# Kernel optimization log

Measured on AMD Instinct MI355X. Metric: run time of the kernel, lower is better.

Reference implementation:

```python
import jax, jax.numpy as jnp
import numpy as np

N, K, D = 65536, 8192, 256

def setup_inputs() -> dict:
    key = jax.random.key(0)
    k1, k2 = jax.random.split(key)
    z = jax.random.normal(k1, (N, D), dtype=jnp.float32)
    # torch init: uniform(-1/K, 1/K)
    emb_w = jax.random.uniform(k2, (K, D), dtype=jnp.float32, minval=-1.0 / K, maxval=1.0 / K)
    return {"z": z, "emb_w": emb_w}

def reference(z, emb_w):
    # distance[n,k] = ||z_n||^2 + ||e_k||^2 - 2 z_n . e_k  (argmin is gradient-free)
    z2 = jnp.sum(z * z, axis=1, keepdims=True)            # [N,1]
    e2 = jnp.sum(emb_w * emb_w, axis=1)                    # [K]
    distance = z2 + e2 - 2.0 * (z @ emb_w.T)               # [N,K]
    indices = jnp.argmin(distance, axis=-1)                # [N]
    quantized = emb_w[indices]                             # [N,D]
    straight_through = jax.lax.stop_gradient(quantized - z) + z
    return quantized, straight_through, indices
```

## Files before the change

### kernel.cpp

```cpp
#include <hip/hip_runtime.h>
#include <hip/hip_fp16.h>

#define N_TOK 65536
#define K_EMB 8192
#define D_DIM 256
#define LIST_CAP 12288
#define CAND_CAP 16384

typedef unsigned short u16;
typedef unsigned int u32;
typedef unsigned long long u64;
typedef _Float16 f16x8 __attribute__((ext_vector_type(8)));
typedef float f32x16 __attribute__((ext_vector_type(16)));

__device__ __forceinline__ u16 f2h(float f) {
  union { _Float16 h; u16 u; } c; c.h = (_Float16)f; return c.u;
}
__device__ __forceinline__ f16x8 as_f16x8(uint4 v) {
  union { uint4 u; f16x8 h; } c; c.u = v; return c.h;
}
__device__ __forceinline__ void gld_lds16(const u16* g, u16* l) {
  __builtin_amdgcn_global_load_lds((const __attribute__((address_space(1))) void*)g,
                                   (__attribute__((address_space(3))) void*)l,
                                   16, 0, 0);
}

__global__ void vq_prep(const float* __restrict__ emb, u16* __restrict__ ehh,
                        float* __restrict__ e2f, u16* __restrict__ e2h,
                        int* __restrict__ count, int* __restrict__ candcount) {
  if (blockIdx.x == 0 && threadIdx.x == 0) { *count = 0; *candcount = 0; }
  const int w = threadIdx.x >> 6, lane = threadIdx.x & 63;
  const int k = blockIdx.x * 4 + w;
  const float4 v = ((const float4*)(emb + (size_t)k * D_DIM))[lane];
  uint2 p;
  p.x = (u32)f2h(v.x * 524288.0f) | ((u32)f2h(v.y * 524288.0f) << 16);
  p.y = (u32)f2h(v.z * 524288.0f) | ((u32)f2h(v.w * 524288.0f) << 16);
  ((uint2*)(ehh + (size_t)k * D_DIM))[lane] = p;
  double s = (double)v.x * v.x + (double)v.y * v.y +
             (double)v.z * v.z + (double)v.w * v.w;
  #pragma unroll
  for (int off = 32; off > 0; off >>= 1) s += __shfl_down(s, off);
  if (lane == 0) { e2f[k] = (float)s; e2h[k] = f2h(-(float)s * 16777216.0f); }
}

__global__ void vq_z2(const float* __restrict__ zg, float* __restrict__ z2f) {
  const int w = threadIdx.x >> 6, lane = threadIdx.x & 63;
  const int n = blockIdx.x * 4 + w;
  const float4 v = ((const float4*)(zg + (size_t)n * D_DIM))[lane];
  double s = (double)v.x * v.x + (double)v.y * v.y +
             (double)v.z * v.z + (double)v.w * v.w;
  #pragma unroll
  for (int off = 32; off > 0; off >>= 1) s += __shfl_down(s, off);
  if (lane == 0) z2f[n] = (float)s;
}

__launch_bounds__(512, 4)
__global__ void vq_phase1(const float* __restrict__ zg, const u16* __restrict__ ehh,
                          const u16* __restrict__ e2h, const float* __restrict__ z2f,
                          int* __restrict__ idx1_ws, int* __restrict__ thrbuf,
                          u64* __restrict__ refbuf, int* __restrict__ list,
                          int* __restrict__ count) {
  __shared__ u16 lds[2][16384];

  const int tid  = threadIdx.x;
  const int w    = tid >> 6;
  const int lane = tid & 63;
  const int q    = w & 1;
  const int g    = w >> 1;
  const int col  = lane & 31;
  const int h    = lane >> 5;
  const int n0   = blockIdx.x * 128 + g * 32;

  uint4 zres[16];
  {
    const float4* zp = (const float4*)(zg + (size_t)(n0 + col) * D_DIM);
    #pragma unroll
    for (int c = 0; c < 16; ++c) {
      float4 a = zp[c * 4 + h * 2];
      float4 b = zp[c * 4 + h * 2 + 1];
      uint4 u;
      u.x = (u32)f2h(a.x * 64.0f) | ((u32)f2h(a.y * 64.0f) << 16);
      u.y = (u32)f2h(a.z * 64.0f) | ((u32)f2h(a.w * 64.0f) << 16);
      u.z = (u32)f2h(b.x * 64.0f) | ((u32)f2h(b.y * 64.0f) << 16);
      u.w = (u32)f2h(b.z * 64.0f) | ((u32)f2h(b.w * 64.0f) << 16);
      zres[c] = u;
    }
  }
  uint4 bone = {0, 0, 0, 0};
  if (h == 0) bone.x = 0x3C00u;

  int m1 = (int)0x80000000, m2 = (int)0x80000000;

  #pragma unroll
  for (int i = 0; i < 4; ++i) {
    int pp = w * 4 + i, qs = pp >> 4, cs = pp & 15;
    gld_lds16(ehh + (size_t)(qs * 32 + col) * D_DIM + cs * 16 + h * 8,
              &lds[0][qs * 8192 + cs * 512]);
  }

  for (int t = 0; t < 128; ++t) {
    const int b = t & 1;
    __syncthreads();
    if (t + 1 < 128) {
      const int nb = b ^ 1, kb2 = (t + 1) * 64;
      #pragma unroll
      for (int i = 0; i < 4; ++i) {
        int pp = w * 4 + i, qs = pp >> 4, cs = pp & 15;
        gld_lds16(ehh + (size_t)(kb2 + qs * 32 + col) * D_DIM + cs * 16 + h * 8,
                  &lds[nb][qs * 8192 + cs * 512]);
      }
    }
    const int kb = t * 64 + q * 32;
    uint4 ea = {0, 0, 0, 0};
    if (h == 0) ea.x = (u32)e2h[kb + col];

    const u16* lb = &lds[b][q * 8192];
    f32x16 acc = {};
    #pragma unroll
    for (int c = 0; c < 16; ++c) {
      f16x8 a = as_f16x8(*(const uint4*)(lb + c * 512 + lane * 8));
      acc = __builtin_amdgcn_mfma_f32_32x32x16_f16(a, as_f16x8(zres[c]), acc, 0, 0, 0);
    }
    acc = __builtin_amdgcn_mfma_f32_32x32x16_f16(as_f16x8(ea), as_f16x8(bone), acc, 0, 0, 0);

    const int base_inv = 4095 - t * 32 - q * 16;
    #pragma unroll
    for (int r = 0; r < 16; ++r) {
      int key = ((int)acc[r] << 12) + (base_inv - r);
      m2 = max(m2, min(m1, key));
      m1 = max(m1, key);
    }
  }

  int k1;
  {
    int x = 4095 - (m1 & 4095);
    int kt = x >> 5, kq = (x >> 4) & 1, kr = x & 15;
    k1 = kt * 64 + kq * 32 + (kr & 3) + 8 * (kr >> 2) + 4 * h;
    int o1 = __shfl_xor(m1, 32), o2 = __shfl_xor(m2, 32);
    int ok1 = __shfl_xor(k1, 32);
    bool take = (o1 > m1) || (o1 == m1 && ok1 < k1);
    int loser = take ? m1 : o1;
    if (take) { m1 = o1; k1 = ok1; }
    m2 = max(m2, max(o2, loser));
  }

  __syncthreads();
  int* rm1 = (int*)&lds[0][0];
  int* rk1 = (int*)&lds[0][1024];
  int* rm2 = (int*)&lds[0][2048];
  if (lane < 32) {
    int nl = q * 128 + g * 32 + col;
    rm1[nl] = m1; rk1[nl] = k1; rm2[nl] = m2;
  }
  __syncthreads();
  if (tid < 128) {
    int a1 = rm1[tid], a2 = rm2[tid], ak = rk1[tid];
    int c1 = rm1[128 + tid], c2 = rm2[128 + tid], ck = rk1[128 + tid];
    bool take = (c1 > a1) || (c1 == a1 && ck < ak);
    int M1 = take ? c1 : a1;
    int K1 = take ? ck : ak;
    int M2 = max(max(a2, c2), take ? a1 : c1);
    int n = blockIdx.x * 128 + tid;
    int M1a = M1 >> 12, M2a = M2 >> 12;
    int e = (int)((__float_as_uint(z2f[n] + 0.01f) >> 23) & 255);
    e = min(max(e, 127), 140);
    int bin = 1 << (e - 126);
    int p = 0;
    if ((M1a - M2a) < (bin * 2 + 128)) {
      int pos = atomicAdd(count, 1);
      if (pos < LIST_CAP) {
        list[pos] = n;
        thrbuf[pos] = M1a - (bin + 256);
        refbuf[pos] = 0xFFFFFFFFFFFFFFFFULL;
        p = pos + 1;
      }
    }
    idx1_ws[n] = K1 | (p << 13);
  }
}

__launch_bounds__(512, 2)
__global__ void vq_cand(const float* __restrict__ zg, const u16* __restrict__ ehh,
                        const u16* __restrict__ e2h, const int* __restrict__ count,
                        const int* __restrict__ list, const int* __restrict__ thrbuf,
                        u32* __restrict__ candbuf, int* __restrict__ candcount) {
  __shared__ u16 lds[2][32768];
  int cnt = *count; if (cnt > LIST_CAP) cnt = LIST_CAP;
  const int tile = blockIdx.x;
  if (tile * 64 >= cnt) return;
  const int tid = threadIdx.x, w = tid >> 6, lane = tid & 63;
  const int q = w & 3, g = w >> 2;
  const int col = lane & 31, h = lane >> 5;
  const int ct = tile * 64 + g * 32 + col;
  const bool valid = ct < cnt;
  const int n_tok = valid ? (list[ct] & (N_TOK - 1)) : 0;
  const int thr = valid ? thrbuf[ct] : 0x7FFFFFFF;

  uint4 zres[16];
  {
    const float4* zp = (const float4*)(zg + (size_t)n_tok * D_DIM);
    #pragma unroll
    for (int c = 0; c < 16; ++c) {
      float4 a = zp[c * 4 + h * 2];
      float4 b2 = zp[c * 4 + h * 2 + 1];
      uint4 u;
      u.x = (u32)f2h(a.x * 64.0f) | ((u32)f2h(a.y * 64.0f) << 16);
      u.y = (u32)f2h(a.z * 64.0f) | ((u32)f2h(a.w * 64.0f) << 16);
      u.z = (u32)f2h(b2.x * 64.0f) | ((u32)f2h(b2.y * 64.0f) << 16);
      u.w = (u32)f2h(b2.z * 64.0f) | ((u32)f2h(b2.w * 64.0f) << 16);
      zres[c] = u;
    }
  }
  uint4 bone = {0, 0, 0, 0};
  if (h == 0) bone.x = 0x3C00u;

  #pragma unroll
  for (int i = 0; i < 8; ++i) {
    int p2 = w * 8 + i, qs = p2 >> 4, cs = p2 & 15;
    gld_lds16(ehh + (size_t)(qs * 32 + col) * D_DIM + cs * 16 + h * 8,
              &lds[0][qs * 8192 + cs * 512]);
  }

  for (int tK = 0; tK < 64; ++tK) {
    const int b = tK & 1;
    __syncthreads();
    if (tK + 1 < 64) {
      const int nb = b ^ 1, kb2 = (tK + 1) * 128;
      #pragma unroll
      for (int i = 0; i < 8; ++i) {
        int p2 = w * 8 + i, qs = p2 >> 4, cs = p2 & 15;
        gld_lds16(ehh + (size_t)(kb2 + qs * 32 + col) * D_DIM + cs * 16 + h * 8,
                  &lds[nb][qs * 8192 + cs * 512]);
      }
    }
    const int kb = tK * 128 + q * 32;
    uint4 ea = {0, 0, 0, 0};
    if (h == 0) ea.x = (u32)e2h[kb + col];
    const u16* lb = &lds[b][q * 8192];
    f32x16 acc = {};
    #pragma unroll
    for (int c = 0; c < 16; ++c) {
      f16x8 a = as_f16x8(*(const uint4*)(lb + c * 512 + lane * 8));
      acc = __builtin_amdgcn_mfma_f32_32x32x16_f16(a, as_f16x8(zres[c]), acc, 0, 0, 0);
    }
    acc = __builtin_amdgcn_mfma_f32_32x32x16_f16(as_f16x8(ea), as_f16x8(bone), acc, 0, 0, 0);
    #pragma unroll
    for (int r = 0; r < 16; ++r) {
      if ((int)acc[r] >= thr) {
        int kg = kb + (r & 3) + 8 * (r >> 2) + 4 * h;
        int pos = atomicAdd(candcount, 1);
        if (pos < CAND_CAP) candbuf[pos] = ((u32)ct << 13) | (u32)kg;
      }
    }
  }
}

__global__ void vq_refine2(const float* __restrict__ zg, const float* __restrict__ emb,
                           const float* __restrict__ z2f, const float* __restrict__ e2f,
                           const int* __restrict__ list, const int* __restrict__ candcount,
                           const u32* __restrict__ candbuf, u64* __restrict__ refbuf) {
  const int w = threadIdx.x >> 6, lane = threadIdx.x & 63;
  int ccnt = *candcount; if (ccnt > CAND_CAP) ccnt = CAND_CAP;
  for (int i = blockIdx.x * 4 + w; i < ccnt; i += gridDim.x * 4) {
    const u32 rec = candbuf[i];
    const int p = (int)(rec >> 13), k = (int)(rec & 8191u);
    const int n = list[p] & (N_TOK - 1);
    float4 zv = ((const float4*)(zg + (size_t)n * D_DIM))[lane];
    float4 ev = ((const float4*)(emb + (size_t)k * D_DIM))[lane];
    double s = (double)zv.x * ev.x + (double)zv.y * ev.y +
               (double)zv.z * ev.z + (double)zv.w * ev.w;
    #pragma unroll
    for (int off = 32; off > 0; off >>= 1) s += __shfl_down(s, off);
    if (lane == 0) {
      float S = z2f[n] + e2f[k];
      float val = S - 2.0f * (float)s;
      u64 key = ((u64)__float_as_uint(val) << 13) | (u64)k;
      atomicMin((unsigned long long*)(refbuf + p), (unsigned long long)key);
    }
  }
}

__global__ void vq_gather(const float* __restrict__ emb, const int* __restrict__ idx1_ws,
                          const u64* __restrict__ refbuf, float* __restrict__ out) {
  const int w = threadIdx.x >> 6, lane = threadIdx.x & 63;
  const int n = blockIdx.x * 4 + w;
  const int enc = idx1_ws[n];
  int idx = enc & 8191;
  const int p = enc >> 13;
  if (p > 0) {
    u64 rb = refbuf[p - 1];
    if (rb != 0xFFFFFFFFFFFFFFFFULL) idx = (int)(rb & 8191ULL);
  }
  float4 v = ((const float4*)(emb + (size_t)idx * D_DIM))[lane];
  float4* o = (float4*)out;
  o[(size_t)n * 64 + lane] = v;
  o[(size_t)4194304 + (size_t)n * 64 + lane] = v;
  if (lane == 0) out[(size_t)33554432 + n] = (float)idx;
}

extern "C" void kernel_launch(void* const* d_in, const int* in_sizes, int n_in,
                              void* d_out, int out_size, void* d_ws, size_t ws_size,
                              hipStream_t stream) {
  const float* z   = (const float*)d_in[0];
  const float* emb = (const float*)d_in[1];
  char* ws = (char*)d_ws;
  u16*   ehh       = (u16*)(ws);
  float* e2f       = (float*)(ws + 4194304);
  u16*   e2h       = (u16*)(ws + 4227072);
  float* z2f       = (float*)(ws + 4243456);
  int*   idx1_ws   = (int*)(ws + 4505600);
  u64*   refbuf    = (u64*)(ws + 4767744);
  int*   list      = (int*)(ws + 4866048);
  int*   thrbuf    = (int*)(ws + 4915200);
  u32*   candbuf   = (u32*)(ws + 4964352);
  int*   count     = (int*)(ws + 5029888);
  int*   candcount = (int*)(ws + 5029892);

  vq_prep   <<<K_EMB / 4, 256, 0, stream>>>(emb, ehh, e2f, e2h, count, candcount);
  vq_z2     <<<N_TOK / 4, 256, 0, stream>>>(z, z2f);
  vq_phase1 <<<N_TOK / 128, 512, 0, stream>>>(z, ehh, e2h, z2f, idx1_ws, thrbuf,
                                              refbuf, list, count);
  vq_cand   <<<256, 512, 0, stream>>>(z, ehh, e2h, count, list, thrbuf,
                                      candbuf, candcount);
  vq_refine2<<<256, 256, 0, stream>>>(z, emb, z2f, e2f, list, candcount,
                                      candbuf, refbuf);
  vq_gather <<<N_TOK / 4, 256, 0, stream>>>(emb, idx1_ws, refbuf, (float*)d_out);
}
```

Before: 742.4 us.

## Fuse z-norm into phase1, software-pipeline its MFMA loop, split candidate K range

Removes the separate vq_z2 kernel by computing each token's squared norm in double while phase1 loads z. The norm is kept in LDS for the threshold test and also written to global memory for refine. The phase1 main loop now alternates two accumulators, so the argmax scan of one tile overlaps the MFMAs of the next. vq_cand splits the codebook into four K slices per row tile, raising its grid from 256 to 768 blocks, and refine2's grid is doubled. These changes add parallelism and cut a launch, at the cost of higher register pressure in phase1 and redundant z conversion across the K-split blocks.

```diff
diff --git a/kernel.cpp b/kernel.cpp
--- a/kernel.cpp
+++ b/kernel.cpp
@@ -43,24 +43,14 @@
   if (lane == 0) { e2f[k] = (float)s; e2h[k] = f2h(-(float)s * 16777216.0f); }
 }
 
-__global__ void vq_z2(const float* __restrict__ zg, float* __restrict__ z2f) {
-  const int w = threadIdx.x >> 6, lane = threadIdx.x & 63;
-  const int n = blockIdx.x * 4 + w;
-  const float4 v = ((const float4*)(zg + (size_t)n * D_DIM))[lane];
-  double s = (double)v.x * v.x + (double)v.y * v.y +
-             (double)v.z * v.z + (double)v.w * v.w;
-  #pragma unroll
-  for (int off = 32; off > 0; off >>= 1) s += __shfl_down(s, off);
-  if (lane == 0) z2f[n] = (float)s;
-}
-
 __launch_bounds__(512, 4)
 __global__ void vq_phase1(const float* __restrict__ zg, const u16* __restrict__ ehh,
-                          const u16* __restrict__ e2h, const float* __restrict__ z2f,
+                          const u16* __restrict__ e2h, float* __restrict__ z2f,
                           int* __restrict__ idx1_ws, int* __restrict__ thrbuf,
                           u64* __restrict__ refbuf, int* __restrict__ list,
                           int* __restrict__ count) {
   __shared__ u16 lds[2][16384];
+  __shared__ float z2s[128];
 
   const int tid  = threadIdx.x;
   const int w    = tid >> 6;
@@ -72,12 +62,17 @@
   const int n0   = blockIdx.x * 128 + g * 32;
 
   uint4 zres[16];
+  double zs = 0.0;
   {
     const float4* zp = (const float4*)(zg + (size_t)(n0 + col) * D_DIM);
     #pragma unroll
     for (int c = 0; c < 16; ++c) {
       float4 a = zp[c * 4 + h * 2];
       float4 b = zp[c * 4 + h * 2 + 1];
+      zs += (double)a.x * a.x + (double)a.y * a.y +
+            (double)a.z * a.z + (double)a.w * a.w;
+      zs += (double)b.x * b.x + (double)b.y * b.y +
+            (double)b.z * b.z + (double)b.w * b.w;
       uint4 u;
       u.x = (u32)f2h(a.x * 64.0f) | ((u32)f2h(a.y * 64.0f) << 16);
       u.y = (u32)f2h(a.z * 64.0f) | ((u32)f2h(a.w * 64.0f) << 16);
@@ -86,51 +81,74 @@
       zres[c] = u;
     }
   }
+  zs += __shfl_xor(zs, 32);
+  if (lane < 32) {
+    z2s[g * 32 + col] = (float)zs;
+    z2f[n0 + col] = (float)zs;
+  }
+
   uint4 bone = {0, 0, 0, 0};
   if (h == 0) bone.x = 0x3C00u;
 
   int m1 = (int)0x80000000, m2 = (int)0x80000000;
-
-  #pragma unroll
-  for (int i = 0; i < 4; ++i) {
-    int pp = w * 4 + i, qs = pp >> 4, cs = pp & 15;
-    gld_lds16(ehh + (size_t)(qs * 32 + col) * D_DIM + cs * 16 + h * 8,
-              &lds[0][qs * 8192 + cs * 512]);
-  }
-
-  for (int t = 0; t < 128; ++t) {
-    const int b = t & 1;
+  f32x16 accA = {}, accB = {};
+
+#define P1_STAGE(TT, BUF) { \
+    _Pragma("unroll") \
+    for (int i = 0; i < 4; ++i) { \
+      int pp = w * 4 + i, qs = pp >> 4, cs = pp & 15; \
+      gld_lds16(ehh + (size_t)((TT) * 64 + qs * 32 + col) * D_DIM + cs * 16 + h * 8, \
+                &lds[BUF][qs * 8192 + cs * 512]); \
+    } }
+#define P1_COMPUTE(ACC, TT, BUF) { \
+    const int kb_ = (TT) * 64 + q * 32; \
+    uint4 ea_ = {0, 0, 0, 0}; \
+    if (h == 0) ea_.x = (u32)e2h[kb_ + col]; \
+    const u16* lb_ = &lds[BUF][q * 8192]; \
+    _Pragma("unroll") \
+    for (int c = 0; c < 16; ++c) { \
+      f16x8 a_ = as_f16x8(*(const uint4*)(lb_ + c * 512 + lane * 8)); \
+      ACC = __builtin_amdgcn_mfma_f32_32x32x16_f16(a_, as_f16x8(zres[c]), ACC, 0, 0, 0); \
+    } \
+    ACC = __builtin_amdgcn_mfma_f32_32x32x16_f16(as_f16x8(ea_), as_f16x8(bone), ACC, 0, 0, 0); }
+#define P1_SCAN(ACC, TT) { \
+    const int base_inv_ = 4095 - (TT) * 32 - q * 16; \
+    _Pragma("unroll") \
+    for (int r = 0; r < 16; ++r) { \
+      int key_ = ((int)ACC[r] << 12) + (base_inv_ - r); \
+      m2 = max(m2, min(m1, key_)); \
+      m1 = max(m1, key_); \
+    } }
+#define P1_ZERO(ACC) { \
+    _Pragma("unroll") \
+    for (int r = 0; r < 16; ++r) ACC[r] = 0.0f; }
+
+  P1_STAGE(0, 0);
+  __syncthreads();
+  P1_STAGE(1, 1);
+  P1_COMPUTE(accA, 0, 0);
+
+  for (int t = 1; t < 127; t += 2) {
     __syncthreads();
-    if (t + 1 < 128) {
-      const int nb = b ^ 1, kb2 = (t + 1) * 64;
-      #pragma unroll
-      for (int i = 0; i < 4; ++i) {
-        int pp = w * 4 + i, qs = pp >> 4, cs = pp & 15;
-        gld_lds16(ehh + (size_t)(kb2 + qs * 32 + col) * D_DIM + cs * 16 + h * 8,
-                  &lds[nb][qs * 8192 + cs * 512]);
-      }
-    }
-    const int kb = t * 64 + q * 32;
-    uint4 ea = {0, 0, 0, 0};
-    if (h == 0) ea.x = (u32)e2h[kb + col];
-
-    const u16* lb = &lds[b][q * 8192];
-    f32x16 acc = {};
-    #pragma unroll
-    for (int c = 0; c < 16; ++c) {
-      f16x8 a = as_f16x8(*(const uint4*)(lb + c * 512 + lane * 8));
-      acc = __builtin_amdgcn_mfma_f32_32x32x16_f16(a, as_f16x8(zres[c]), acc, 0, 0, 0);
-    }
-    acc = __builtin_amdgcn_mfma_f32_32x32x16_f16(as_f16x8(ea), as_f16x8(bone), acc, 0, 0, 0);
-
-    const int base_inv = 4095 - t * 32 - q * 16;
-    #pragma unroll
-    for (int r = 0; r < 16; ++r) {
-      int key = ((int)acc[r] << 12) + (base_inv - r);
-      m2 = max(m2, min(m1, key));
-      m1 = max(m1, key);
-    }
-  }
+    P1_STAGE(t + 1, (t + 1) & 1);
+    P1_COMPUTE(accB, t, t & 1);
+    P1_SCAN(accA, t - 1);
+    P1_ZERO(accA);
+    __syncthreads();
+    P1_STAGE(t + 2, (t + 2) & 1);
+    P1_COMPUTE(accA, t + 1, (t + 1) & 1);
+    P1_SCAN(accB, t);
+    P1_ZERO(accB);
+  }
+  __syncthreads();
+  P1_COMPUTE(accB, 127, 1);
+  P1_SCAN(accA, 126);
+  P1_SCAN(accB, 127);
+
+#undef P1_STAGE
+#undef P1_COMPUTE
+#undef P1_SCAN
+#undef P1_ZERO
 
   int k1;
   {
@@ -163,7 +181,7 @@
     int M2 = max(max(a2, c2), take ? a1 : c1);
     int n = blockIdx.x * 128 + tid;
     int M1a = M1 >> 12, M2a = M2 >> 12;
-    int e = (int)((__float_as_uint(z2f[n] + 0.01f) >> 23) & 255);
+    int e = (int)((__float_as_uint(z2s[tid] + 0.01f) >> 23) & 255);
     e = min(max(e, 127), 140);
     int bin = 1 << (e - 126);
     int p = 0;
@@ -187,12 +205,14 @@
                         u32* __restrict__ candbuf, int* __restrict__ candcount) {
   __shared__ u16 lds[2][32768];
   int cnt = *count; if (cnt > LIST_CAP) cnt = LIST_CAP;
-  const int tile = blockIdx.x;
-  if (tile * 64 >= cnt) return;
+  const int rt = blockIdx.x >> 2;
+  const int ks = blockIdx.x & 3;
+  if (rt * 64 >= cnt) return;
+  const int k0 = ks * 2048;
   const int tid = threadIdx.x, w = tid >> 6, lane = tid & 63;
   const int q = w & 3, g = w >> 2;
   const int col = lane & 31, h = lane >> 5;
-  const int ct = tile * 64 + g * 32 + col;
+  const int ct = rt * 64 + g * 32 + col;
   const bool valid = ct < cnt;
   const int n_tok = valid ? (list[ct] & (N_TOK - 1)) : 0;
   const int thr = valid ? thrbuf[ct] : 0x7FFFFFFF;
@@ -218,15 +238,15 @@
   #pragma unroll
   for (int i = 0; i < 8; ++i) {
     int p2 = w * 8 + i, qs = p2 >> 4, cs = p2 & 15;
-    gld_lds16(ehh + (size_t)(qs * 32 + col) * D_DIM + cs * 16 + h * 8,
+    gld_lds16(ehh + (size_t)(k0 + qs * 32 + col) * D_DIM + cs * 16 + h * 8,
               &lds[0][qs * 8192 + cs * 512]);
   }
 
-  for (int tK = 0; tK < 64; ++tK) {
+  for (int tK = 0; tK < 16; ++tK) {
     const int b = tK & 1;
     __syncthreads();
-    if (tK + 1 < 64) {
-      const int nb = b ^ 1, kb2 = (tK + 1) * 128;
+    if (tK + 1 < 16) {
+      const int nb = b ^ 1, kb2 = k0 + (tK + 1) * 128;
       #pragma unroll
       for (int i = 0; i < 8; ++i) {
         int p2 = w * 8 + i, qs = p2 >> 4, cs = p2 & 15;
@@ -234,7 +254,7 @@
                   &lds[nb][qs * 8192 + cs * 512]);
       }
     }
-    const int kb = tK * 128 + q * 32;
+    const int kb = k0 + tK * 128 + q * 32;
     uint4 ea = {0, 0, 0, 0};
     if (h == 0) ea.x = (u32)e2h[kb + col];
     const u16* lb = &lds[b][q * 8192];
@@ -318,12 +338,11 @@
   int*   candcount = (int*)(ws + 5029892);
 
   vq_prep   <<<K_EMB / 4, 256, 0, stream>>>(emb, ehh, e2f, e2h, count, candcount);
-  vq_z2     <<<N_TOK / 4, 256, 0, stream>>>(z, z2f);
   vq_phase1 <<<N_TOK / 128, 512, 0, stream>>>(z, ehh, e2h, z2f, idx1_ws, thrbuf,
                                               refbuf, list, count);
-  vq_cand   <<<256, 512, 0, stream>>>(z, ehh, e2h, count, list, thrbuf,
+  vq_cand   <<<768, 512, 0, stream>>>(z, ehh, e2h, count, list, thrbuf,
                                       candbuf, candcount);
-  vq_refine2<<<256, 256, 0, stream>>>(z, emb, z2f, e2f, list, candcount,
+  vq_refine2<<<512, 256, 0, stream>>>(z, emb, z2f, e2f, list, candcount,
                                       candbuf, refbuf);
   vq_gather <<<N_TOK / 4, 256, 0, stream>>>(emb, idx1_ws, refbuf, (float*)d_out);
 }
```

Result: slower. 881.3 us (+18.7%).

## Make phase1 codebook-stationary with K-sliced partials and a merge pass

Applied to the files above, without the earlier changes.

Phase1 now has each block hold a 128-code slice of the fp16 codebook in LDS once. Blocks stream precomputed fp16 token rows and write per-slice top-2 partials to scratch, and a new merge kernel reduces them and builds the candidate list. This replaces the per-block double-buffered streaming of the whole codebook and the in-loop fp32→fp16 conversion of z. The candidate kernel is also split four ways over K for more parallelism, and the refine grid is enlarged. The trade-off is tens of MB of partial traffic, written into the output buffer as scratch, plus one extra launch.

```diff
diff --git a/kernel.cpp b/kernel.cpp
--- a/kernel.cpp
+++ b/kernel.cpp
@@ -6,6 +6,8 @@
 #define D_DIM 256
 #define LIST_CAP 12288
 #define CAND_CAP 16384
+#define NSLICE 64
+#define KSLICE 128
 
 typedef unsigned short u16;
 typedef unsigned int u32;
@@ -43,10 +45,15 @@
   if (lane == 0) { e2f[k] = (float)s; e2h[k] = f2h(-(float)s * 16777216.0f); }
 }
 
-__global__ void vq_z2(const float* __restrict__ zg, float* __restrict__ z2f) {
+__global__ void vq_zprep(const float* __restrict__ zg, u16* __restrict__ zhh,
+                         float* __restrict__ z2f) {
   const int w = threadIdx.x >> 6, lane = threadIdx.x & 63;
   const int n = blockIdx.x * 4 + w;
   const float4 v = ((const float4*)(zg + (size_t)n * D_DIM))[lane];
+  uint2 p;
+  p.x = (u32)f2h(v.x * 64.0f) | ((u32)f2h(v.y * 64.0f) << 16);
+  p.y = (u32)f2h(v.z * 64.0f) | ((u32)f2h(v.w * 64.0f) << 16);
+  ((uint2*)(zhh + (size_t)n * D_DIM))[lane] = p;
   double s = (double)v.x * v.x + (double)v.y * v.y +
              (double)v.z * v.z + (double)v.w * v.w;
   #pragma unroll
@@ -54,130 +61,121 @@
   if (lane == 0) z2f[n] = (float)s;
 }
 
-__launch_bounds__(512, 4)
-__global__ void vq_phase1(const float* __restrict__ zg, const u16* __restrict__ ehh,
-                          const u16* __restrict__ e2h, const float* __restrict__ z2f,
-                          int* __restrict__ idx1_ws, int* __restrict__ thrbuf,
-                          u64* __restrict__ refbuf, int* __restrict__ list,
-                          int* __restrict__ count) {
-  __shared__ u16 lds[2][16384];
+__launch_bounds__(512, 2)
+__global__ void vq_phase1(const u16* __restrict__ zhh, const u16* __restrict__ ehh,
+                          const u16* __restrict__ e2h,
+                          int* __restrict__ pm1, u32* __restrict__ pk,
+                          int* __restrict__ pm2) {
+  __shared__ u16 lds[32768];
 
   const int tid  = threadIdx.x;
   const int w    = tid >> 6;
   const int lane = tid & 63;
-  const int q    = w & 1;
-  const int g    = w >> 1;
   const int col  = lane & 31;
   const int h    = lane >> 5;
-  const int n0   = blockIdx.x * 128 + g * 32;
-
-  uint4 zres[16];
-  {
-    const float4* zp = (const float4*)(zg + (size_t)(n0 + col) * D_DIM);
-    #pragma unroll
-    for (int c = 0; c < 16; ++c) {
-      float4 a = zp[c * 4 + h * 2];
-      float4 b = zp[c * 4 + h * 2 + 1];
-      uint4 u;
-      u.x = (u32)f2h(a.x * 64.0f) | ((u32)f2h(a.y * 64.0f) << 16);
-      u.y = (u32)f2h(a.z * 64.0f) | ((u32)f2h(a.w * 64.0f) << 16);
-      u.z = (u32)f2h(b.x * 64.0f) | ((u32)f2h(b.y * 64.0f) << 16);
-      u.w = (u32)f2h(b.z * 64.0f) | ((u32)f2h(b.w * 64.0f) << 16);
-      zres[c] = u;
-    }
-  }
+  const int slice = blockIdx.x & (NSLICE - 1);
+  const int chunk = blockIdx.x >> 6;
+  const int k0    = slice * KSLICE;
+  const int nbase = chunk * 16384;
+
+  #pragma unroll
+  for (int i = 0; i < 8; ++i) {
+    int pp = w * 8 + i, qs = pp >> 4, cs = pp & 15;
+    gld_lds16(ehh + (size_t)(k0 + qs * 32 + col) * D_DIM + cs * 16 + h * 8,
+              &lds[qs * 8192 + cs * 512]);
+  }
+
   uint4 bone = {0, 0, 0, 0};
   if (h == 0) bone.x = 0x3C00u;
-
-  int m1 = (int)0x80000000, m2 = (int)0x80000000;
-
-  #pragma unroll
-  for (int i = 0; i < 4; ++i) {
-    int pp = w * 4 + i, qs = pp >> 4, cs = pp & 15;
-    gld_lds16(ehh + (size_t)(qs * 32 + col) * D_DIM + cs * 16 + h * 8,
-              &lds[0][qs * 8192 + cs * 512]);
-  }
-
-  for (int t = 0; t < 128; ++t) {
-    const int b = t & 1;
-    __syncthreads();
-    if (t + 1 < 128) {
-      const int nb = b ^ 1, kb2 = (t + 1) * 64;
+  uint4 ea[4] = {{0,0,0,0},{0,0,0,0},{0,0,0,0},{0,0,0,0}};
+  #pragma unroll
+  for (int kt = 0; kt < 4; ++kt)
+    if (h == 0) ea[kt].x = (u32)e2h[k0 + kt * 32 + col];
+
+  __syncthreads();
+
+  for (int it = 0; it < 64; ++it) {
+    const int n0 = nbase + it * 256 + w * 32;
+    const uint4* zp = (const uint4*)(zhh + (size_t)(n0 + col) * D_DIM);
+    uint4 zres[16];
+    #pragma unroll
+    for (int c = 0; c < 16; ++c) zres[c] = zp[c * 2 + h];
+
+    f32x16 acc[4] = {};
+    #pragma unroll
+    for (int c = 0; c < 16; ++c) {
+      f16x8 zb = as_f16x8(zres[c]);
       #pragma unroll
-      for (int i = 0; i < 4; ++i) {
-        int pp = w * 4 + i, qs = pp >> 4, cs = pp & 15;
-        gld_lds16(ehh + (size_t)(kb2 + qs * 32 + col) * D_DIM + cs * 16 + h * 8,
-                  &lds[nb][qs * 8192 + cs * 512]);
+      for (int kt = 0; kt < 4; ++kt) {
+        f16x8 a = as_f16x8(*(const uint4*)(&lds[kt * 8192 + c * 512 + lane * 8]));
+        acc[kt] = __builtin_amdgcn_mfma_f32_32x32x16_f16(a, zb, acc[kt], 0, 0, 0);
       }
     }
-    const int kb = t * 64 + q * 32;
-    uint4 ea = {0, 0, 0, 0};
-    if (h == 0) ea.x = (u32)e2h[kb + col];
-
-    const u16* lb = &lds[b][q * 8192];
-    f32x16 acc = {};
-    #pragma unroll
-    for (int c = 0; c < 16; ++c) {
-      f16x8 a = as_f16x8(*(const uint4*)(lb + c * 512 + lane * 8));
-      acc = __builtin_amdgcn_mfma_f32_32x32x16_f16(a, as_f16x8(zres[c]), acc, 0, 0, 0);
-    }
-    acc = __builtin_amdgcn_mfma_f32_32x32x16_f16(as_f16x8(ea), as_f16x8(bone), acc, 0, 0, 0);
-
-    const int base_inv = 4095 - t * 32 - q * 16;
-    #pragma unroll
-    for (int r = 0; r < 16; ++r) {
-      int key = ((int)acc[r] << 12) + (base_inv - r);
-      m2 = max(m2, min(m1, key));
-      m1 = max(m1, key);
-    }
-  }
-
-  int k1;
-  {
-    int x = 4095 - (m1 & 4095);
-    int kt = x >> 5, kq = (x >> 4) & 1, kr = x & 15;
-    k1 = kt * 64 + kq * 32 + (kr & 3) + 8 * (kr >> 2) + 4 * h;
+    #pragma unroll
+    for (int kt = 0; kt < 4; ++kt)
+      acc[kt] = __builtin_amdgcn_mfma_f32_32x32x16_f16(as_f16x8(ea[kt]),
+                                                       as_f16x8(bone), acc[kt], 0, 0, 0);
+
+    int m1 = (int)0x80000000, m2 = (int)0x80000000;
+    #pragma unroll
+    for (int kt = 0; kt < 4; ++kt) {
+      const int base_inv = 127 - kt * 32;
+      #pragma unroll
+      for (int r = 0; r < 16; ++r) {
+        int key = ((int)acc[kt][r] << 12) + (base_inv - ((r & 3) + 8 * (r >> 2)));
+        m2 = max(m2, min(m1, key));
+        m1 = max(m1, key);
+      }
+    }
+    int pos = 127 - (m1 & 4095);
+    int k1 = k0 + pos + 4 * h;
     int o1 = __shfl_xor(m1, 32), o2 = __shfl_xor(m2, 32);
     int ok1 = __shfl_xor(k1, 32);
     bool take = (o1 > m1) || (o1 == m1 && ok1 < k1);
     int loser = take ? m1 : o1;
     if (take) { m1 = o1; k1 = ok1; }
     m2 = max(m2, max(o2, loser));
-  }
-
-  __syncthreads();
-  int* rm1 = (int*)&lds[0][0];
-  int* rk1 = (int*)&lds[0][1024];
-  int* rm2 = (int*)&lds[0][2048];
-  if (lane < 32) {
-    int nl = q * 128 + g * 32 + col;
-    rm1[nl] = m1; rk1[nl] = k1; rm2[nl] = m2;
-  }
-  __syncthreads();
-  if (tid < 128) {
-    int a1 = rm1[tid], a2 = rm2[tid], ak = rk1[tid];
-    int c1 = rm1[128 + tid], c2 = rm2[128 + tid], ck = rk1[128 + tid];
-    bool take = (c1 > a1) || (c1 == a1 && ck < ak);
-    int M1 = take ? c1 : a1;
-    int K1 = take ? ck : ak;
-    int M2 = max(max(a2, c2), take ? a1 : c1);
-    int n = blockIdx.x * 128 + tid;
-    int M1a = M1 >> 12, M2a = M2 >> 12;
-    int e = (int)((__float_as_uint(z2f[n] + 0.01f) >> 23) & 255);
-    e = min(max(e, 127), 140);
-    int bin = 1 << (e - 126);
-    int p = 0;
-    if ((M1a - M2a) < (bin * 2 + 128)) {
-      int pos = atomicAdd(count, 1);
-      if (pos < LIST_CAP) {
-        list[pos] = n;
-        thrbuf[pos] = M1a - (bin + 256);
-        refbuf[pos] = 0xFFFFFFFFFFFFFFFFULL;
-        p = pos + 1;
-      }
-    }
-    idx1_ws[n] = K1 | (p << 13);
-  }
+
+    if (lane < 32) {
+      size_t idx = (size_t)slice * N_TOK + (n0 + col);
+      pm1[idx] = m1 >> 12;
+      pk[idx]  = (u32)k1;
+      pm2[idx] = m2 >> 12;
+    }
+  }
+}
+
+__global__ void vq_merge(const float* __restrict__ z2f, const int* __restrict__ pm1,
+                         const u32* __restrict__ pk, const int* __restrict__ pm2,
+                         int* __restrict__ idx1_ws, int* __restrict__ thrbuf,
+                         u64* __restrict__ refbuf, int* __restrict__ list,
+                         int* __restrict__ count) {
+  const int n = blockIdx.x * 256 + threadIdx.x;
+  int M1 = (int)0x80000000, K1 = 0x7FFFFFFF, M2 = (int)0x80000000;
+  #pragma unroll 8
+  for (int s = 0; s < NSLICE; ++s) {
+    size_t idx = (size_t)s * N_TOK + n;
+    int a = pm1[idx];
+    int k = (int)pk[idx];
+    int b = pm2[idx];
+    bool take = (a > M1) || (a == M1 && k < K1);
+    if (take) { M2 = max(M2, M1); M1 = a; K1 = k; M2 = max(M2, b); }
+    else      { M2 = max(M2, a); }
+  }
+  int e = (int)((__float_as_uint(z2f[n] + 0.01f) >> 23) & 255);
+  e = min(max(e, 127), 140);
+  int bin = 1 << (e - 126);
+  int p = 0;
+  if ((M1 - M2) < (bin * 2 + 128)) {
+    int pos = atomicAdd(count, 1);
+    if (pos < LIST_CAP) {
+      list[pos] = n;
+      thrbuf[pos] = M1 - (bin + 256);
+      refbuf[pos] = 0xFFFFFFFFFFFFFFFFULL;
+      p = pos + 1;
+    }
+  }
+  idx1_ws[n] = K1 | (p << 13);
 }
 
 __launch_bounds__(512, 2)
@@ -187,12 +185,14 @@
                         u32* __restrict__ candbuf, int* __restrict__ candcount) {
   __shared__ u16 lds[2][32768];
   int cnt = *count; if (cnt > LIST_CAP) cnt = LIST_CAP;
-  const int tile = blockIdx.x;
-  if (tile * 64 >= cnt) return;
+  const int rt = blockIdx.x >> 2;
+  const int ks = blockIdx.x & 3;
+  if (rt * 64 >= cnt) return;
+  const int k0 = ks * 2048;
   const int tid = threadIdx.x, w = tid >> 6, lane = tid & 63;
   const int q = w & 3, g = w >> 2;
   const int col = lane & 31, h = lane >> 5;
-  const int ct = tile * 64 + g * 32 + col;
+  const int ct = rt * 64 + g * 32 + col;
   const bool valid = ct < cnt;
   const int n_tok = valid ? (list[ct] & (N_TOK - 1)) : 0;
   const int thr = valid ? thrbuf[ct] : 0x7FFFFFFF;
@@ -218,15 +218,15 @@
   #pragma unroll
   for (int i = 0; i < 8; ++i) {
     int p2 = w * 8 + i, qs = p2 >> 4, cs = p2 & 15;
-    gld_lds16(ehh + (size_t)(qs * 32 + col) * D_DIM + cs * 16 + h * 8,
+    gld_lds16(ehh + (size_t)(k0 + qs * 32 + col) * D_DIM + cs * 16 + h * 8,
               &lds[0][qs * 8192 + cs * 512]);
   }
 
-  for (int tK = 0; tK < 64; ++tK) {
+  for (int tK = 0; tK < 16; ++tK) {
     const int b = tK & 1;
     __syncthreads();
-    if (tK + 1 < 64) {
-      const int nb = b ^ 1, kb2 = (tK + 1) * 128;
+    if (tK + 1 < 16) {
+      const int nb = b ^ 1, kb2 = k0 + (tK + 1) * 128;
       #pragma unroll
       for (int i = 0; i < 8; ++i) {
         int p2 = w * 8 + i, qs = p2 >> 4, cs = p2 & 15;
@@ -234,7 +234,7 @@
                   &lds[nb][qs * 8192 + cs * 512]);
       }
     }
-    const int kb = tK * 128 + q * 32;
+    const int kb = k0 + tK * 128 + q * 32;
     uint4 ea = {0, 0, 0, 0};
     if (h == 0) ea.x = (u32)e2h[kb + col];
     const u16* lb = &lds[b][q * 8192];
@@ -317,13 +317,20 @@
   int*   count     = (int*)(ws + 5029888);
   int*   candcount = (int*)(ws + 5029892);
 
+  char* ob = (char*)d_out;
+  u16*  zhh = (u16*)(ob);
+  int*  pm1 = (int*)(ob + 33554432);
+  u32*  pkb = (u32*)(ob + 50331648);
+  int*  pm2 = (int*)(ob + 67108864);
+
   vq_prep   <<<K_EMB / 4, 256, 0, stream>>>(emb, ehh, e2f, e2h, count, candcount);
-  vq_z2     <<<N_TOK / 4, 256, 0, stream>>>(z, z2f);
-  vq_phase1 <<<N_TOK / 128, 512, 0, stream>>>(z, ehh, e2h, z2f, idx1_ws, thrbuf,
+  vq_zprep  <<<N_TOK / 4, 256, 0, stream>>>(z, zhh, z2f);
+  vq_phase1 <<<256, 512, 0, stream>>>(zhh, ehh, e2h, pm1, pkb, pm2);
+  vq_merge  <<<N_TOK / 256, 256, 0, stream>>>(z2f, pm1, pkb, pm2, idx1_ws, thrbuf,
                                               refbuf, list, count);
-  vq_cand   <<<256, 512, 0, stream>>>(z, ehh, e2h, count, list, thrbuf,
+  vq_cand   <<<768, 512, 0, stream>>>(z, ehh, e2h, count, list, thrbuf,
                                       candbuf, candcount);
-  vq_refine2<<<256, 256, 0, stream>>>(z, emb, z2f, e2f, list, candcount,
+  vq_refine2<<<512, 256, 0, stream>>>(z, emb, z2f, e2f, list, candcount,
                                       candbuf, refbuf);
   vq_gather <<<N_TOK / 4, 256, 0, stream>>>(emb, idx1_ws, refbuf, (float*)d_out);
 }
```

Result: slower. 1.151 ms (+55.0%).
